# Optimization experiments

Hardware: AMD Instinct MI355X
Metric: run time of the kernel (lower is better)

Reference implementation:

```python
import jax, jax.numpy as jnp
import numpy as np

STRIDE = (2, 2)
PADDING = ((1, 1), (1, 1))


def setup_inputs() -> dict:
    key = jax.random.key(0)
    k1, k2, k3, k4 = jax.random.split(key, 4)
    B, Cin, H, W = 32, 128, 112, 112
    Cout, E, kh, kw = 256, 4, 3, 3
    x = jax.random.normal(k1, (B, Cin, H, W), dtype=jnp.float32)
    routing_w = jax.random.normal(k2, (E, Cin), dtype=jnp.float32) * (1.0 / np.sqrt(Cin))
    routing_b = jax.random.normal(k3, (E,), dtype=jnp.float32) * 0.01
    expert_weight = jax.random.normal(k4, (E, Cout, Cin, kh, kw), dtype=jnp.float32) * (1.0 / np.sqrt(Cin * kh * kw))
    return {"x": x, "routing_w": routing_w, "routing_b": routing_b, "expert_weight": expert_weight}


def reference(x, routing_w, routing_b, expert_weight):
    # Routing: global average pool -> linear -> sigmoid  (B, E)
    pooled = jnp.mean(x, axis=(2, 3))
    rw = jax.nn.sigmoid(pooled @ routing_w.T + routing_b)
    # Per-sample dynamic kernels: (B, Cout, Cin, kh, kw)
    kernels = jnp.einsum('be,eoihw->boihw', rw, expert_weight)

    def conv_one(xi, wi):
        # xi: (Cin, H, W), wi: (Cout, Cin, kh, kw)
        return jax.lax.conv_general_dilated(
            xi[None], wi, window_strides=STRIDE, padding=PADDING,
            dimension_numbers=('NCHW', 'OIHW', 'NCHW'))[0]

    return jax.vmap(conv_one)(x, kernels)
```

## Files before the change

kernel.cpp:

```cpp
#include <hip/hip_runtime.h>
#include <cstdint>

typedef unsigned short u16;
typedef unsigned int u32;

typedef __attribute__((ext_vector_type(8))) short bf16x8;
typedef __attribute__((ext_vector_type(4))) float f32x4;

#define KDIM 1152
#define MDIM 256
#define NPIX 3136
#define PLANE 12544
#define EWSTRIDE 294912
#define HH 114
#define XT_SAMP ((size_t)HH * HH * 128)

__device__ __forceinline__ u16 f2bf(float f) {
  u32 u = __float_as_uint(f);
  return (u16)((u + 0x7FFFu + ((u >> 16) & 1u)) >> 16);
}

__device__ __forceinline__ void gl_lds16(const u16* g, u16* l) {
  __builtin_amdgcn_global_load_lds((__attribute__((address_space(1))) void*)g,
                                   (__attribute__((address_space(3))) void*)l,
                                   16, 0, 0);
}

__global__ __launch_bounds__(256) void halo_kernel(u16* __restrict__ xt) {
  const int b = blockIdx.x;
  u32* xg = (u32*)xt + (size_t)b * (HH * HH * 64);
  for (int idx = threadIdx.x; idx < 452 * 64; idx += 256) {
    const int pix = idx >> 6, c = idx & 63;
    int h, w;
    if (pix < 114) { h = 0; w = pix; }
    else if (pix < 228) { h = 113; w = pix - 114; }
    else { const int q = pix - 228; h = 1 + (q >> 1); w = (q & 1) ? 113 : 0; }
    xg[((size_t)h * HH + w) * 64 + c] = 0u;
  }
}

__global__ __launch_bounds__(256) void transpose_pool_kernel(
    const float* __restrict__ x, u16* __restrict__ xt, float* __restrict__ part) {
  __shared__ u32 tile[112 * 68];
  __shared__ float psum[512];
  const int h = blockIdx.x, b = blockIdx.y;
  const int t = threadIdx.x, lane = t & 63, wave = t >> 6;
  const float* xb = x + (size_t)b * 128 * PLANE + h * 112;
  if (lane < 56) {
    #pragma unroll
    for (int wh = 0; wh < 2; ++wh) {
      const int w = wh * 56 + lane;
      #pragma unroll
      for (int i = 0; i < 4; ++i) {
        const int ci0 = (i * 4 + wave) * 8;
        const float* p = xb + (size_t)ci0 * PLANE + w;
        float v0 = p[0];
        float v1 = p[(size_t)1 * PLANE];
        float v2 = p[(size_t)2 * PLANE];
        float v3 = p[(size_t)3 * PLANE];
        float v4 = p[(size_t)4 * PLANE];
        float v5 = p[(size_t)5 * PLANE];
        float v6 = p[(size_t)6 * PLANE];
        float v7 = p[(size_t)7 * PLANE];
        uint4 d;
        d.x = (u32)f2bf(v0) | ((u32)f2bf(v1) << 16);
        d.y = (u32)f2bf(v2) | ((u32)f2bf(v3) << 16);
        d.z = (u32)f2bf(v4) | ((u32)f2bf(v5) << 16);
        d.w = (u32)f2bf(v6) | ((u32)f2bf(v7) << 16);
        *(uint4*)&tile[w * 68 + ci0 / 2] = d;
      }
    }
  }
  __syncthreads();
  const int c = t & 63;
  float s0 = 0.f, s1 = 0.f;
  u32* xg = (u32*)xt + (((size_t)b * HH + h + 1) * HH + 1) * 64;
  #pragma unroll
  for (int j = 0; j < 28; ++j) {
    const int idx = t + 256 * j;
    const int w = idx >> 6;
    const u32 v = tile[w * 68 + c];
    s0 += __uint_as_float(v << 16);
    s1 += __uint_as_float(v & 0xffff0000u);
    xg[(size_t)w * 64 + c] = v;
  }
  psum[wave * 128 + 2 * c] = s0;
  psum[wave * 128 + 2 * c + 1] = s1;
  __syncthreads();
  if (t < 128)
    part[((size_t)h * 32 + b) * 128 + t] =
        psum[t] + psum[128 + t] + psum[256 + t] + psum[384 + t];
}

__global__ void reduce_pool_kernel(const float* __restrict__ part,
                                   float* __restrict__ pooled) {
  const int b = blockIdx.x, t = threadIdx.x;
  float s = 0.f;
  for (int h = 0; h < 112; ++h) s += part[((size_t)h * 32 + b) * 128 + t];
  pooled[b * 128 + t] = s;
}

__global__ void routing_kernel(const float* __restrict__ pooled,
                               const float* __restrict__ rww,
                               const float* __restrict__ rwb,
                               float* __restrict__ rw, float scale) {
  const int t = threadIdx.x;
  if (t >= 128) return;
  const int b = t >> 2, e = t & 3;
  float acc = rwb[e];
  for (int c = 0; c < 128; ++c) acc += pooled[b * 128 + c] * scale * rww[e * 128 + c];
  rw[b * 4 + e] = 1.0f / (1.0f + expf(-acc));
}

__global__ __launch_bounds__(256) void mix_kernel(const float* __restrict__ ew,
                                                  const float* __restrict__ rw,
                                                  u16* __restrict__ wmix) {
  const int t = threadIdx.x;
  const int oc = blockIdx.x * 4 + (t >> 6);
  const int lane = t & 63;
  const int b0 = blockIdx.y * 8;
  float ereg[4][18];
  #pragma unroll
  for (int e = 0; e < 4; ++e) {
    const float* p = ew + ((size_t)e * 256 + oc) * 1152 + lane * 18;
    #pragma unroll
    for (int j = 0; j < 18; ++j) ereg[e][j] = p[j];
  }
  for (int bb = 0; bb < 8; ++bb) {
    const int b = b0 + bb;
    const float w0 = rw[b * 4 + 0], w1 = rw[b * 4 + 1];
    const float w2 = rw[b * 4 + 2], w3 = rw[b * 4 + 3];
    u32* dst = (u32*)(wmix + ((size_t)b * 256 + oc) * KDIM) + lane;
    #pragma unroll
    for (int r = 0; r < 9; ++r) {
      const float va = w0 * ereg[0][r] + w1 * ereg[1][r] + w2 * ereg[2][r] + w3 * ereg[3][r];
      const float vb = w0 * ereg[0][9 + r] + w1 * ereg[1][9 + r] + w2 * ereg[2][9 + r] + w3 * ereg[3][9 + r];
      dst[r * 64] = (u32)f2bf(va) | ((u32)f2bf(vb) << 16);
    }
  }
}

__global__ __launch_bounds__(256) void gemm_kernel(const u16* __restrict__ wmix,
                                                   const u16* __restrict__ xt,
                                                   float* __restrict__ out) {
  __shared__ u16 a_sm[128 * 32];
  __shared__ u16 b_sm[128 * 32];
  const int b = blockIdx.x;
  const int mt = blockIdx.y & 1, nt = blockIdx.y >> 1;
  const int tid = threadIdx.x, lane = tid & 63, wave = tid >> 6;
  const int srow = lane >> 2, scol = (lane & 3) * 8;
  const u16* ga0 = wmix + (size_t)b * EWSTRIDE + (size_t)(mt * 128 + wave * 16 + srow) * KDIM + scol;
  const u16* ga1 = ga0 + 64 * KDIM;
  u16* la0 = a_sm + wave * 512 + lane * 8;
  u16* la1 = la0 + 2048;
  const u16* xtb = xt + (size_t)b * XT_SAMP;
  int p0 = nt * 128 + wave * 16 + (lane >> 2);
  int p1 = p0 + 64;
  if (p0 > NPIX - 1) p0 = NPIX - 1;
  if (p1 > NPIX - 1) p1 = NPIX - 1;
  const size_t pb0 = ((size_t)(2 * (p0 / 56)) * HH + 2 * (p0 % 56)) * 128 + scol;
  const size_t pb1 = ((size_t)(2 * (p1 / 56)) * HH + 2 * (p1 % 56)) * 128 + scol;
  u16* lb0 = b_sm + wave * 512 + lane * 8;
  u16* lb1 = lb0 + 2048;

  const int wm = wave >> 1, wn = wave & 1;
  const int fr = lane & 15, quad = lane >> 4;
  f32x4 acc[4][4];
  const f32x4 zv = {0.f, 0.f, 0.f, 0.f};
  #pragma unroll
  for (int i = 0; i < 4; ++i)
    #pragma unroll
    for (int j = 0; j < 4; ++j) acc[i][j] = zv;

  for (int kt = 0; kt < 36; ++kt) {
    const int r = kt >> 2;
    const size_t toff = (size_t)((r / 3) * HH + (r % 3)) * 128 + (kt & 3) * 32;
    gl_lds16(ga0, la0);
    gl_lds16(ga1, la1);
    gl_lds16(xtb + pb0 + toff, lb0);
    gl_lds16(xtb + pb1 + toff, lb1);
    ga0 += 32; ga1 += 32;
    __syncthreads();
    bf16x8 av[4], bv[4];
    #pragma unroll
    for (int i = 0; i < 4; ++i)
      av[i] = *(const bf16x8*)(a_sm + (wm * 64 + i * 16 + fr) * 32 + quad * 8);
    #pragma unroll
    for (int j = 0; j < 4; ++j)
      bv[j] = *(const bf16x8*)(b_sm + (wn * 64 + j * 16 + fr) * 32 + quad * 8);
    #pragma unroll
    for (int i = 0; i < 4; ++i)
      #pragma unroll
      for (int j = 0; j < 4; ++j)
        acc[i][j] = __builtin_amdgcn_mfma_f32_16x16x32_bf16(av[i], bv[j], acc[i][j], 0, 0, 0);
    __syncthreads();
  }

  float* os = out + (size_t)b * MDIM * NPIX;
  const int mbase = mt * 128 + wm * 64 + quad * 4;
  const int nb = nt * 128 + wn * 64 + fr;
  #pragma unroll
  for (int j = 0; j < 4; ++j) {
    const int n = nb + j * 16;
    if (n < NPIX) {
      #pragma unroll
      for (int i = 0; i < 4; ++i) {
        const int m = mbase + i * 16;
        #pragma unroll
        for (int rr = 0; rr < 4; ++rr)
          os[(size_t)(m + rr) * NPIX + n] = acc[i][j][rr];
      }
    }
  }
}

__global__ __launch_bounds__(256) void pool_kernel(const float* __restrict__ x,
                                                   float* __restrict__ pooled) {
  const int ci = blockIdx.x, b = blockIdx.y;
  const float4* p = (const float4*)(x + ((size_t)b * 128 + ci) * PLANE);
  float s = 0.f;
  for (int i = threadIdx.x; i < PLANE / 4; i += 256) {
    float4 v = p[i];
    s += v.x + v.y + v.z + v.w;
  }
  #pragma unroll
  for (int off = 32; off > 0; off >>= 1) s += __shfl_down(s, off, 64);
  __shared__ float red[4];
  if ((threadIdx.x & 63) == 0) red[threadIdx.x >> 6] = s;
  __syncthreads();
  if (threadIdx.x == 0)
    pooled[b * 128 + ci] = (red[0] + red[1] + red[2] + red[3]) * (1.0f / (float)PLANE);
}

__global__ __launch_bounds__(256) void naive_conv(const float* __restrict__ x,
                                                  const float* __restrict__ ew,
                                                  const float* __restrict__ rw,
                                                  float* __restrict__ out) {
  const size_t idx = (size_t)blockIdx.x * 256 + threadIdx.x;
  if (idx >= (size_t)32 * MDIM * NPIX) return;
  const int n = (int)(idx % NPIX);
  const int tmp = (int)(idx / NPIX);
  const int oc = tmp % MDIM;
  const int b = tmp / MDIM;
  const int oh = n / 56, ow = n % 56;
  const float w0 = rw[b * 4 + 0], w1 = rw[b * 4 + 1];
  const float w2 = rw[b * 4 + 2], w3 = rw[b * 4 + 3];
  float acc = 0.f;
  for (int ci = 0; ci < 128; ++ci) {
    const float* xp = x + ((size_t)b * 128 + ci) * PLANE;
    const size_t wb = ((size_t)oc * 128 + ci) * 9;
    for (int kh = 0; kh < 3; ++kh) {
      const int ih = 2 * oh - 1 + kh;
      if (ih < 0 || ih >= 112) continue;
      for (int kw = 0; kw < 3; ++kw) {
        const int iw = 2 * ow - 1 + kw;
        if (iw < 0 || iw >= 112) continue;
        const int ko = kh * 3 + kw;
        const float wsum = w0 * ew[wb + ko] + w1 * ew[(size_t)EWSTRIDE + wb + ko]
                         + w2 * ew[2 * (size_t)EWSTRIDE + wb + ko]
                         + w3 * ew[3 * (size_t)EWSTRIDE + wb + ko];
        acc += xp[ih * 112 + iw] * wsum;
      }
    }
  }
  out[idx] = acc;
}

extern "C" void kernel_launch(void* const* d_in, const int* in_sizes, int n_in,
                              void* d_out, int out_size, void* d_ws, size_t ws_size,
                              hipStream_t stream) {
  const float* x   = (const float*)d_in[0];
  const float* rww = (const float*)d_in[1];
  const float* rwb = (const float*)d_in[2];
  const float* ew  = (const float*)d_in[3];
  float* out = (float*)d_out;

  const size_t xt_bytes = 32 * XT_SAMP * 2;
  const size_t wmix_off = xt_bytes;
  const size_t part_off = wmix_off + (size_t)32 * EWSTRIDE * 2;
  const size_t pooled_off = part_off + (size_t)112 * 32 * 128 * 4;
  const size_t rw_off = pooled_off + 16384;
  const size_t need = rw_off + 512;

  if (ws_size >= need) {
    u16* xt = (u16*)d_ws;
    u16* wmix = (u16*)((char*)d_ws + wmix_off);
    float* part = (float*)((char*)d_ws + part_off);
    float* pooled = (float*)((char*)d_ws + pooled_off);
    float* rw_ws = (float*)((char*)d_ws + rw_off);
    halo_kernel<<<32, 256, 0, stream>>>(xt);
    transpose_pool_kernel<<<dim3(112, 32), 256, 0, stream>>>(x, xt, part);
    reduce_pool_kernel<<<32, 128, 0, stream>>>(part, pooled);
    routing_kernel<<<1, 128, 0, stream>>>(pooled, rww, rwb, rw_ws, 1.0f / (float)PLANE);
    mix_kernel<<<dim3(64, 4), 256, 0, stream>>>(ew, rw_ws, wmix);
    gemm_kernel<<<dim3(32, 50), 256, 0, stream>>>(wmix, xt, out);
  } else {
    float* pooled = (float*)d_ws;
    float* rw_ws = (float*)((char*)d_ws + 16384);
    pool_kernel<<<dim3(128, 32), 256, 0, stream>>>(x, pooled);
    routing_kernel<<<1, 128, 0, stream>>>(pooled, rww, rwb, rw_ws, 1.0f);
    naive_conv<<<(int)(((size_t)32 * MDIM * NPIX + 255) / 256), 256, 0, stream>>>(
        x, ew, rw_ws, out);
  }
}
```

Baseline: 459.6 us.

## Fuse halo zeroing and routing into neighbors, load two K-slices per GEMM sync

Halo zeroing moves into the transpose kernel, and the pool reduction is fused with routing into one kernel, removing two launches. The mix kernel's grid doubles, with each block handling 4 samples instead of 8. The GEMM now loads two 32-wide K-chunks into separate LDS buffers before each barrier, halving the number of sync pairs. This is not true double-buffering, since loads still do not overlap compute, and LDS use doubles.

```diff
diff --git a/kernel.cpp b/kernel.cpp
--- a/kernel.cpp
+++ b/kernel.cpp
@@ -26,25 +26,25 @@
                                    16, 0, 0);
 }
 
-__global__ __launch_bounds__(256) void halo_kernel(u16* __restrict__ xt) {
-  const int b = blockIdx.x;
-  u32* xg = (u32*)xt + (size_t)b * (HH * HH * 64);
-  for (int idx = threadIdx.x; idx < 452 * 64; idx += 256) {
-    const int pix = idx >> 6, c = idx & 63;
-    int h, w;
-    if (pix < 114) { h = 0; w = pix; }
-    else if (pix < 228) { h = 113; w = pix - 114; }
-    else { const int q = pix - 228; h = 1 + (q >> 1); w = (q & 1) ? 113 : 0; }
-    xg[((size_t)h * HH + w) * 64 + c] = 0u;
-  }
-}
-
 __global__ __launch_bounds__(256) void transpose_pool_kernel(
     const float* __restrict__ x, u16* __restrict__ xt, float* __restrict__ part) {
   __shared__ u32 tile[112 * 68];
   __shared__ float psum[512];
   const int h = blockIdx.x, b = blockIdx.y;
   const int t = threadIdx.x, lane = t & 63, wave = t >> 6;
+
+  {
+    u32* xrow = (u32*)xt + ((size_t)b * HH + (h + 1)) * HH * 64;
+    if (t < 128) {
+      const int w = (t >= 64) ? 113 : 0;
+      xrow[(size_t)w * 64 + (t & 63)] = 0u;
+    }
+    if (h == 0 || h == 111) {
+      u32* xr = (u32*)xt + ((size_t)b * HH + (h == 0 ? 0 : 113)) * HH * 64;
+      for (int i = t; i < HH * 64; i += 256) xr[i] = 0u;
+    }
+  }
+
   const float* xb = x + (size_t)b * 128 * PLANE + h * 112;
   if (lane < 56) {
     #pragma unroll
@@ -92,12 +92,147 @@
         psum[t] + psum[128 + t] + psum[256 + t] + psum[384 + t];
 }
 
-__global__ void reduce_pool_kernel(const float* __restrict__ part,
-                                   float* __restrict__ pooled) {
+__global__ __launch_bounds__(256) void reduce_routing_kernel(
+    const float* __restrict__ part, const float* __restrict__ rww,
+    const float* __restrict__ rwb, float* __restrict__ rw) {
+  __shared__ float red[256];
+  __shared__ float pl[128];
   const int b = blockIdx.x, t = threadIdx.x;
+  const int ci = t & 127, half = t >> 7;
   float s = 0.f;
-  for (int h = 0; h < 112; ++h) s += part[((size_t)h * 32 + b) * 128 + t];
-  pooled[b * 128 + t] = s;
+  const float* p = part + ((size_t)(half * 56) * 32 + b) * 128 + ci;
+  #pragma unroll 4
+  for (int h = 0; h < 56; ++h) s += p[(size_t)h * 32 * 128];
+  red[t] = s;
+  __syncthreads();
+  if (t < 128) pl[t] = red[t] + red[t + 128];
+  __syncthreads();
+  const int e = t >> 6, l = t & 63;
+  float acc = pl[l] * rww[e * 128 + l] + pl[l + 64] * rww[e * 128 + l + 64];
+  #pragma unroll
+  for (int off = 32; off > 0; off >>= 1) acc += __shfl_down(acc, off, 64);
+  if (l == 0) {
+    const float logit = acc * (1.0f / (float)PLANE) + rwb[e];
+    rw[b * 4 + e] = 1.0f / (1.0f + expf(-logit));
+  }
+}
+
+__global__ __launch_bounds__(256) void mix_kernel(const float* __restrict__ ew,
+                                                  const float* __restrict__ rw,
+                                                  u16* __restrict__ wmix) {
+  const int t = threadIdx.x;
+  const int oc = blockIdx.x * 4 + (t >> 6);
+  const int lane = t & 63;
+  const int b0 = blockIdx.y * 4;
+  float ereg[4][18];
+  #pragma unroll
+  for (int e = 0; e < 4; ++e) {
+    const float* p = ew + ((size_t)e * 256 + oc) * 1152 + lane * 18;
+    #pragma unroll
+    for (int j = 0; j < 18; ++j) ereg[e][j] = p[j];
+  }
+  for (int bb = 0; bb < 4; ++bb) {
+    const int b = b0 + bb;
+    const float w0 = rw[b * 4 + 0], w1 = rw[b * 4 + 1];
+    const float w2 = rw[b * 4 + 2], w3 = rw[b * 4 + 3];
+    u32* dst = (u32*)(wmix + ((size_t)b * 256 + oc) * KDIM) + lane;
+    #pragma unroll
+    for (int r = 0; r < 9; ++r) {
+      const float va = w0 * ereg[0][r] + w1 * ereg[1][r] + w2 * ereg[2][r] + w3 * ereg[3][r];
+      const float vb = w0 * ereg[0][9 + r] + w1 * ereg[1][9 + r] + w2 * ereg[2][9 + r] + w3 * ereg[3][9 + r];
+      dst[r * 64] = (u32)f2bf(va) | ((u32)f2bf(vb) << 16);
+    }
+  }
+}
+
+__global__ __launch_bounds__(256) void gemm_kernel(const u16* __restrict__ wmix,
+                                                   const u16* __restrict__ xt,
+                                                   float* __restrict__ out) {
+  __shared__ u16 a_sm[2][128 * 32];
+  __shared__ u16 b_sm[2][128 * 32];
+  const int b = blockIdx.x;
+  const int mt = blockIdx.y & 1, nt = blockIdx.y >> 1;
+  const int tid = threadIdx.x, lane = tid & 63, wave = tid >> 6;
+  const int srow = lane >> 2, scol = (lane & 3) * 8;
+  const u16* ga0 = wmix + (size_t)b * EWSTRIDE + (size_t)(mt * 128 + wave * 16 + srow) * KDIM + scol;
+  const u16* ga1 = ga0 + 64 * KDIM;
+  const u16* xtb = xt + (size_t)b * XT_SAMP;
+  int p0 = nt * 128 + wave * 16 + (lane >> 2);
+  int p1 = p0 + 64;
+  if (p0 > NPIX - 1) p0 = NPIX - 1;
+  if (p1 > NPIX - 1) p1 = NPIX - 1;
+  const size_t pb0 = ((size_t)(2 * (p0 / 56)) * HH + 2 * (p0 % 56)) * 128 + scol;
+  const size_t pb1 = ((size_t)(2 * (p1 / 56)) * HH + 2 * (p1 % 56)) * 128 + scol;
+
+  u16* la00 = &a_sm[0][wave * 512 + lane * 8];
+  u16* la01 = la00 + 2048;
+  u16* la10 = &a_sm[1][wave * 512 + lane * 8];
+  u16* la11 = la10 + 2048;
+  u16* lb00 = &b_sm[0][wave * 512 + lane * 8];
+  u16* lb01 = lb00 + 2048;
+  u16* lb10 = &b_sm[1][wave * 512 + lane * 8];
+  u16* lb11 = lb10 + 2048;
+
+  const int wm = wave >> 1, wn = wave & 1;
+  const int fr = lane & 15, quad = lane >> 4;
+  f32x4 acc[4][4];
+  const f32x4 zv = {0.f, 0.f, 0.f, 0.f};
+  #pragma unroll
+  for (int i = 0; i < 4; ++i)
+    #pragma unroll
+    for (int j = 0; j < 4; ++j) acc[i][j] = zv;
+
+  for (int kt2 = 0; kt2 < 18; ++kt2) {
+    const int k0 = kt2 * 2;
+    const int r = k0 >> 2;
+    const size_t tap = (size_t)((r / 3) * HH + (r % 3)) * 128;
+    const size_t t0 = tap + (size_t)(k0 & 3) * 32;
+    const size_t t1 = t0 + 32;
+    gl_lds16(ga0 + k0 * 32, la00);
+    gl_lds16(ga1 + k0 * 32, la01);
+    gl_lds16(xtb + pb0 + t0, lb00);
+    gl_lds16(xtb + pb1 + t0, lb01);
+    gl_lds16(ga0 + k0 * 32 + 32, la10);
+    gl_lds16(ga1 + k0 * 32 + 32, la11);
+    gl_lds16(xtb + pb0 + t1, lb10);
+    gl_lds16(xtb + pb1 + t1, lb11);
+    __syncthreads();
+    #pragma unroll
+    for (int c = 0; c < 2; ++c) {
+      const u16* as = a_sm[c];
+      const u16* bs = b_sm[c];
+      bf16x8 av[4], bv[4];
+      #pragma unroll
+      for (int i = 0; i < 4; ++i)
+        av[i] = *(const bf16x8*)(as + (wm * 64 + i * 16 + fr) * 32 + quad * 8);
+      #pragma unroll
+      for (int j = 0; j < 4; ++j)
+        bv[j] = *(const bf16x8*)(bs + (wn * 64 + j * 16 + fr) * 32 + quad * 8);
+      #pragma unroll
+      for (int i = 0; i < 4; ++i)
+        #pragma unroll
+        for (int j = 0; j < 4; ++j)
+          acc[i][j] = __builtin_amdgcn_mfma_f32_16x16x32_bf16(av[i], bv[j], acc[i][j], 0, 0, 0);
+    }
+    __syncthreads();
+  }
+
+  float* os = out + (size_t)b * MDIM * NPIX;
+  const int mbase = mt * 128 + wm * 64 + quad * 4;
+  const int nb = nt * 128 + wn * 64 + fr;
+  #pragma unroll
+  for (int j = 0; j < 4; ++j) {
+    const int n = nb + j * 16;
+    if (n < NPIX) {
+      #pragma unroll
+      for (int i = 0; i < 4; ++i) {
+        const int m = mbase + i * 16;
+        #pragma unroll
+        for (int rr = 0; rr < 4; ++rr)
+          os[(size_t)(m + rr) * NPIX + n] = acc[i][j][rr];
+      }
+    }
+  }
 }
 
 __global__ void routing_kernel(const float* __restrict__ pooled,
@@ -110,108 +245,6 @@
   float acc = rwb[e];
   for (int c = 0; c < 128; ++c) acc += pooled[b * 128 + c] * scale * rww[e * 128 + c];
   rw[b * 4 + e] = 1.0f / (1.0f + expf(-acc));
-}
-
-__global__ __launch_bounds__(256) void mix_kernel(const float* __restrict__ ew,
-                                                  const float* __restrict__ rw,
-                                                  u16* __restrict__ wmix) {
-  const int t = threadIdx.x;
-  const int oc = blockIdx.x * 4 + (t >> 6);
-  const int lane = t & 63;
-  const int b0 = blockIdx.y * 8;
-  float ereg[4][18];
-  #pragma unroll
-  for (int e = 0; e < 4; ++e) {
-    const float* p = ew + ((size_t)e * 256 + oc) * 1152 + lane * 18;
-    #pragma unroll
-    for (int j = 0; j < 18; ++j) ereg[e][j] = p[j];
-  }
-  for (int bb = 0; bb < 8; ++bb) {
-    const int b = b0 + bb;
-    const float w0 = rw[b * 4 + 0], w1 = rw[b * 4 + 1];
-    const float w2 = rw[b * 4 + 2], w3 = rw[b * 4 + 3];
-    u32* dst = (u32*)(wmix + ((size_t)b * 256 + oc) * KDIM) + lane;
-    #pragma unroll
-    for (int r = 0; r < 9; ++r) {
-      const float va = w0 * ereg[0][r] + w1 * ereg[1][r] + w2 * ereg[2][r] + w3 * ereg[3][r];
-      const float vb = w0 * ereg[0][9 + r] + w1 * ereg[1][9 + r] + w2 * ereg[2][9 + r] + w3 * ereg[3][9 + r];
-      dst[r * 64] = (u32)f2bf(va) | ((u32)f2bf(vb) << 16);
-    }
-  }
-}
-
-__global__ __launch_bounds__(256) void gemm_kernel(const u16* __restrict__ wmix,
-                                                   const u16* __restrict__ xt,
-                                                   float* __restrict__ out) {
-  __shared__ u16 a_sm[128 * 32];
-  __shared__ u16 b_sm[128 * 32];
-  const int b = blockIdx.x;
-  const int mt = blockIdx.y & 1, nt = blockIdx.y >> 1;
-  const int tid = threadIdx.x, lane = tid & 63, wave = tid >> 6;
-  const int srow = lane >> 2, scol = (lane & 3) * 8;
-  const u16* ga0 = wmix + (size_t)b * EWSTRIDE + (size_t)(mt * 128 + wave * 16 + srow) * KDIM + scol;
-  const u16* ga1 = ga0 + 64 * KDIM;
-  u16* la0 = a_sm + wave * 512 + lane * 8;
-  u16* la1 = la0 + 2048;
-  const u16* xtb = xt + (size_t)b * XT_SAMP;
-  int p0 = nt * 128 + wave * 16 + (lane >> 2);
-  int p1 = p0 + 64;
-  if (p0 > NPIX - 1) p0 = NPIX - 1;
-  if (p1 > NPIX - 1) p1 = NPIX - 1;
-  const size_t pb0 = ((size_t)(2 * (p0 / 56)) * HH + 2 * (p0 % 56)) * 128 + scol;
-  const size_t pb1 = ((size_t)(2 * (p1 / 56)) * HH + 2 * (p1 % 56)) * 128 + scol;
-  u16* lb0 = b_sm + wave * 512 + lane * 8;
-  u16* lb1 = lb0 + 2048;
-
-  const int wm = wave >> 1, wn = wave & 1;
-  const int fr = lane & 15, quad = lane >> 4;
-  f32x4 acc[4][4];
-  const f32x4 zv = {0.f, 0.f, 0.f, 0.f};
-  #pragma unroll
-  for (int i = 0; i < 4; ++i)
-    #pragma unroll
-    for (int j = 0; j < 4; ++j) acc[i][j] = zv;
-
-  for (int kt = 0; kt < 36; ++kt) {
-    const int r = kt >> 2;
-    const size_t toff = (size_t)((r / 3) * HH + (r % 3)) * 128 + (kt & 3) * 32;
-    gl_lds16(ga0, la0);
-    gl_lds16(ga1, la1);
-    gl_lds16(xtb + pb0 + toff, lb0);
-    gl_lds16(xtb + pb1 + toff, lb1);
-    ga0 += 32; ga1 += 32;
-    __syncthreads();
-    bf16x8 av[4], bv[4];
-    #pragma unroll
-    for (int i = 0; i < 4; ++i)
-      av[i] = *(const bf16x8*)(a_sm + (wm * 64 + i * 16 + fr) * 32 + quad * 8);
-    #pragma unroll
-    for (int j = 0; j < 4; ++j)
-      bv[j] = *(const bf16x8*)(b_sm + (wn * 64 + j * 16 + fr) * 32 + quad * 8);
-    #pragma unroll
-    for (int i = 0; i < 4; ++i)
-      #pragma unroll
-      for (int j = 0; j < 4; ++j)
-        acc[i][j] = __builtin_amdgcn_mfma_f32_16x16x32_bf16(av[i], bv[j], acc[i][j], 0, 0, 0);
-    __syncthreads();
-  }
-
-  float* os = out + (size_t)b * MDIM * NPIX;
-  const int mbase = mt * 128 + wm * 64 + quad * 4;
-  const int nb = nt * 128 + wn * 64 + fr;
-  #pragma unroll
-  for (int j = 0; j < 4; ++j) {
-    const int n = nb + j * 16;
-    if (n < NPIX) {
-      #pragma unroll
-      for (int i = 0; i < 4; ++i) {
-        const int m = mbase + i * 16;
-        #pragma unroll
-        for (int rr = 0; rr < 4; ++rr)
-          os[(size_t)(m + rr) * NPIX + n] = acc[i][j][rr];
-      }
-    }
-  }
 }
 
 __global__ __launch_bounds__(256) void pool_kernel(const float* __restrict__ x,
@@ -286,13 +319,10 @@
     u16* xt = (u16*)d_ws;
     u16* wmix = (u16*)((char*)d_ws + wmix_off);
     float* part = (float*)((char*)d_ws + part_off);
-    float* pooled = (float*)((char*)d_ws + pooled_off);
     float* rw_ws = (float*)((char*)d_ws + rw_off);
-    halo_kernel<<<32, 256, 0, stream>>>(xt);
     transpose_pool_kernel<<<dim3(112, 32), 256, 0, stream>>>(x, xt, part);
-    reduce_pool_kernel<<<32, 128, 0, stream>>>(part, pooled);
-    routing_kernel<<<1, 128, 0, stream>>>(pooled, rww, rwb, rw_ws, 1.0f / (float)PLANE);
-    mix_kernel<<<dim3(64, 4), 256, 0, stream>>>(ew, rw_ws, wmix);
+    reduce_routing_kernel<<<32, 256, 0, stream>>>(part, rww, rwb, rw_ws);
+    mix_kernel<<<dim3(64, 8), 256, 0, stream>>>(ew, rw_ws, wmix);
     gemm_kernel<<<dim3(32, 50), 256, 0, stream>>>(wmix, xt, out);
   } else {
     float* pooled = (float*)d_ws;
```

Measured after the change: 443.4 us. -3.5%, faster.
